# Kernel tuning notes

Hardware: AMD Instinct MI355X
Metric: run time of the kernel (lower is better)

The kernel has to match this reference:

```python
import jax, jax.numpy as jnp
import numpy as np

N = 50000
E = 800000
IN_DIM = 128
HID = 128
HEADS = 8
OUT_DIM = 64
LRELU_SLOPE = 0.2


def setup_inputs() -> dict:
    key = jax.random.key(0)
    ks = jax.random.split(key, 10)
    x = jax.random.normal(ks[0], (N, IN_DIM), dtype=jnp.float32)
    edge_index = jax.random.randint(ks[1], (2, E), 0, N, dtype=jnp.int64)
    c1 = HID // HEADS  # 16
    W1 = jax.random.normal(ks[2], (IN_DIM, HID), dtype=jnp.float32) * (1.0 / np.sqrt(IN_DIM))
    as1 = jax.random.normal(ks[3], (HEADS, c1), dtype=jnp.float32) * 0.1
    ad1 = jax.random.normal(ks[4], (HEADS, c1), dtype=jnp.float32) * 0.1
    b1 = jnp.zeros((HID,), dtype=jnp.float32)
    W2 = jax.random.normal(ks[5], (HID, OUT_DIM), dtype=jnp.float32) * (1.0 / np.sqrt(HID))
    as2 = jax.random.normal(ks[6], (1, OUT_DIM), dtype=jnp.float32) * 0.1
    ad2 = jax.random.normal(ks[7], (1, OUT_DIM), dtype=jnp.float32) * 0.1
    b2 = jnp.zeros((OUT_DIM,), dtype=jnp.float32)
    return {"x": x, "edge_index": edge_index, "W1": W1, "as1": as1, "ad1": ad1,
            "b1": b1, "W2": W2, "as2": as2, "ad2": ad2, "b2": b2}


def gat_conv(x, src, dst, W, a_src, a_dst, b, heads, ch, concat):
    n = x.shape[0]
    h = (x @ W).reshape(n, heads, ch)               # [N,H,C]
    alpha_s = jnp.sum(h * a_src, axis=-1)           # [N,H]
    alpha_d = jnp.sum(h * a_dst, axis=-1)           # [N,H]
    e = jax.nn.leaky_relu(alpha_s[src] + alpha_d[dst], LRELU_SLOPE)  # [E,H]
    m = jax.ops.segment_max(e, dst, num_segments=n)  # per-dst max (self-loops guarantee nonempty)
    e = jnp.exp(e - m[dst])
    denom = jax.ops.segment_sum(e, dst, num_segments=n)
    alpha = e / (denom[dst] + 1e-16)                # [E,H]
    msg = h[src] * alpha[:, :, None]                # [E,H,C]
    out = jax.ops.segment_sum(msg, dst, num_segments=n)  # [N,H,C]
    out = out.reshape(n, heads * ch) if concat else out.mean(axis=1)
    return out + b


def reference(x, edge_index, W1, as1, ad1, b1, W2, as2, ad2, b2):
    n = x.shape[0]
    loops = jnp.arange(n, dtype=edge_index.dtype)
    src = jnp.concatenate([edge_index[0], loops])   # PyG GATConv adds self-loops
    dst = jnp.concatenate([edge_index[1], loops])
    # layer 1: GATBlock (dropout is identity at eval), heads=8, concat, ELU
    h = gat_conv(x, src, dst, W1, as1, ad1, b1, HEADS, HID // HEADS, True)
    h = jax.nn.elu(h)
    # final conv: heads=1, concat=False
    out = gat_conv(h, src, dst, W2, as2, ad2, b2, 1, OUT_DIM, False)
    return jax.nn.log_softmax(out, axis=1)
```

## Files before the change

### kernel.cpp

```cpp
#include <hip/hip_runtime.h>
#include <hip/hip_bf16.h>
#include <math.h>

#define IN_DIM 128
#define HID 128
#define HEADS 8
#define OUT_DIM 64
#define SLOPE 0.2f
#define BSHIFT 7
#define BCAP 4096
#define BCAPSHIFT 12
#define EPT 8

typedef short bf16x8 __attribute__((ext_vector_type(8)));
typedef float f32x4 __attribute__((ext_vector_type(4)));

__device__ __forceinline__ float lrelu(float x) { return fmaxf(x, SLOPE * x); }
__device__ __forceinline__ float bf2f(unsigned u) { return __uint_as_float(u << 16); }
__device__ __forceinline__ unsigned short f2bf(float f) {
    unsigned u = __float_as_uint(f);
    return (unsigned short)((u + 0x7FFF + ((u >> 16) & 1)) >> 16);
}

__global__ __launch_bounds__(256) void setup_kernel(
    const float* __restrict__ W1, const float* __restrict__ W2,
    short* __restrict__ w1t, short* __restrict__ w2t, int* __restrict__ gcursor) {
    int t = threadIdx.x;
    int b = blockIdx.x;
    if (b == 96) {
        for (int i = t; i < 512; i += 256) gcursor[i] = 0;
        return;
    }
    if (b < 64) {
        int id = b * 256 + t;
        int n = id >> 7, k = id & 127;
        w1t[id] = (short)f2bf(W1[k * 128 + n]);
    } else {
        int id = (b - 64) * 256 + t;
        int n = id >> 7, k = id & 127;
        w2t[id] = (short)f2bf(W2[k * 64 + n]);
    }
}

__device__ __forceinline__ void bscatter_body(
    int blk, int* smem, const int* __restrict__ idx,
    int* __restrict__ gcursor, unsigned* __restrict__ bucket_buf,
    int E, int N, int NB) {
    int* hist  = smem;
    int* gbase = smem + 512;
    int* lbase = smem + 1024;
    int* wtot  = smem + 1536;
    int* misc  = smem + 1540;
    unsigned* sent = (unsigned*)(smem + 1552);
    unsigned* spos = (unsigned*)(smem + 3600);
    int t = threadIdx.x;
    for (int i = t; i < 512; i += 256) hist[i] = 0;
    if (t == 0) misc[1] = 0;
    __syncthreads();
    {
        int nz = (idx[2 * t + 1] != 0) + (idx[2 * t + 513] != 0);
        if (nz) atomicAdd(&misc[1], nz);
    }
    __syncthreads();
    int flag = (misc[1] > 16) ? 1 : 0;
    int e0 = blk * (256 * EPT);
    int EN = E + N;
    unsigned ent[EPT];
    int bid[EPT];
    int loc[EPT];
#pragma unroll
    for (int k = 0; k < EPT; k++) {
        int e = e0 + k * 256 + t;
        bid[k] = -1;
        if (e < EN) {
            int src, dst;
            if (e < E) {
                if (flag) { src = idx[e]; dst = idx[E + e]; }
                else      { src = idx[2 * e]; dst = idx[2 * (E + e)]; }
            } else {
                src = dst = e - E;
            }
            int b = dst >> BSHIFT;
            bid[k] = b;
            ent[k] = ((unsigned)(dst & ((1 << BSHIFT) - 1)) << 16) | (unsigned)src;
            loc[k] = atomicAdd(&hist[b], 1);
        }
    }
    __syncthreads();
    int i0 = 2 * t;
    int a = hist[i0], b2 = hist[i0 + 1];
    int ps = a + b2;
    int lane = t & 63, w = t >> 6;
    int incl = ps;
#pragma unroll
    for (int off = 1; off < 64; off <<= 1) {
        int u = __shfl_up(incl, off, 64);
        if (lane >= off) incl += u;
    }
    if (lane == 63) wtot[w] = incl;
    __syncthreads();
    int woff = 0;
    for (int k = 0; k < w; k++) woff += wtot[k];
    int ex0 = woff + incl - ps;
    lbase[i0] = ex0;
    lbase[i0 + 1] = ex0 + a;
    if (t == 255) misc[0] = woff + incl;
    for (int i = t; i < 512; i += 256) {
        int c = hist[i];
        gbase[i] = c ? atomicAdd(&gcursor[i], c) : 0;
    }
    __syncthreads();
#pragma unroll
    for (int k = 0; k < EPT; k++) {
        if (bid[k] >= 0) {
            int p = lbase[bid[k]] + loc[k];
            int pib = gbase[bid[k]] + loc[k];
            sent[p] = ent[k];
            spos[p] = (pib < BCAP) ? (((unsigned)bid[k] << BCAPSHIFT) | (unsigned)pib)
                                   : 0xFFFFFFFFu;
        }
    }
    __syncthreads();
    int tot = misc[0];
    for (int i = t; i < tot; i += 256) {
        unsigned sp = spos[i];
        if (sp != 0xFFFFFFFFu) bucket_buf[sp] = sent[i];
    }
}

__device__ __forceinline__ void gemm1_body(
    int blk, char* smemraw, const float* __restrict__ x, const short* __restrict__ w1t,
    const float* __restrict__ a_s, const float* __restrict__ a_d,
    unsigned short* __restrict__ h1g, float* __restrict__ as_n,
    float* __restrict__ ad_n, int N) {
    short* Wt = (short*)smemraw;
    float* hT = (float*)smemraw;
    int t = threadIdx.x;
    const uint4* src = (const uint4*)w1t;
    for (int id = t; id < 128 * 16; id += 256) {
        int n = id >> 4, kg = id & 15;
        *(uint4*)&Wt[n * 128 + ((kg * 8) ^ ((n & 7) << 3))] = src[id];
    }
    __syncthreads();
    int wv = t >> 6, lane = t & 63;
    int m = lane & 15, q = lane >> 4;
    int row = blk * 64 + wv * 16 + m;
    f32x4 acc[8];
#pragma unroll
    for (int j = 0; j < 8; j++) acc[j] = (f32x4){0.f, 0.f, 0.f, 0.f};
    int msw = (m & 7) << 3;
#pragma unroll
    for (int k0 = 0; k0 < 128; k0 += 32) {
        bf16x8 a = {0, 0, 0, 0, 0, 0, 0, 0};
        if (row < N) {
            const float* xp = &x[(size_t)row * 128 + k0 + q * 8];
            float4 u0 = *(const float4*)xp;
            float4 u1 = *(const float4*)(xp + 4);
            a[0] = (short)f2bf(u0.x); a[1] = (short)f2bf(u0.y);
            a[2] = (short)f2bf(u0.z); a[3] = (short)f2bf(u0.w);
            a[4] = (short)f2bf(u1.x); a[5] = (short)f2bf(u1.y);
            a[6] = (short)f2bf(u1.z); a[7] = (short)f2bf(u1.w);
        }
#pragma unroll
        for (int j = 0; j < 8; j++) {
            bf16x8 b = *(const bf16x8*)&Wt[(j * 16 + m) * 128 + ((k0 + q * 8) ^ msw)];
            acc[j] = __builtin_amdgcn_mfma_f32_16x16x32_bf16(a, b, acc[j], 0, 0, 0);
        }
    }
    __syncthreads();
#pragma unroll
    for (int r = 0; r < 4; r++) {
        int rl = wv * 16 + q * 4 + r;
        int sw = ((rl >> 2) & 1) << 4;
        int rb = rl * 128;
#pragma unroll
        for (int j = 0; j < 8; j++)
            hT[rb + ((j * 16 + m) ^ sw)] = acc[j][r];
    }
    __syncthreads();
    int base = blk * 64;
    for (int id = t; id < 1024; id += 256) {
        int rl = id >> 4, c8 = (id & 15) * 8;
        int rg = base + rl;
        if (rg >= N) continue;
        int sw = ((rl >> 2) & 1) << 4;
        float4 u0 = *(const float4*)&hT[rl * 128 + (c8 ^ sw)];
        float4 u1 = *(const float4*)&hT[rl * 128 + ((c8 + 4) ^ sw)];
        uint4 ow;
        ow.x = (unsigned)f2bf(u0.x) | ((unsigned)f2bf(u0.y) << 16);
        ow.y = (unsigned)f2bf(u0.z) | ((unsigned)f2bf(u0.w) << 16);
        ow.z = (unsigned)f2bf(u1.x) | ((unsigned)f2bf(u1.y) << 16);
        ow.w = (unsigned)f2bf(u1.z) | ((unsigned)f2bf(u1.w) << 16);
        *(uint4*)&h1g[(size_t)rg * 128 + c8] = ow;
    }
    for (int it = t; it < 512; it += 256) {
        int rl = it >> 3, hd = it & 7;
        int rg = base + rl;
        int sw = ((rl >> 2) & 1) << 4;
        const float* ap = a_s + hd * 16;
        const float* dp = a_d + hd * 16;
        float s = 0.f, d = 0.f;
#pragma unroll
        for (int p = 0; p < 4; p++) {
            float4 u = *(const float4*)&hT[rl * 128 + ((hd * 16 + p * 4) ^ sw)];
            s += u.x * ap[p * 4] + u.y * ap[p * 4 + 1] + u.z * ap[p * 4 + 2] + u.w * ap[p * 4 + 3];
            d += u.x * dp[p * 4] + u.y * dp[p * 4 + 1] + u.z * dp[p * 4 + 2] + u.w * dp[p * 4 + 3];
        }
        if (rg < N) {
            as_n[(size_t)base * 8 + it] = s;
            ad_n[(size_t)base * 8 + it] = d;
        }
    }
}

__global__ __launch_bounds__(256) void k1_kernel(
    const int* __restrict__ idx, int* __restrict__ gcursor,
    unsigned* __restrict__ bucket_buf,
    const float* __restrict__ x, const short* __restrict__ w1t,
    const float* __restrict__ a_s, const float* __restrict__ a_d,
    unsigned short* __restrict__ h1g, float* __restrict__ as_n,
    float* __restrict__ ad_n, int E, int N, int NB, int GS) {
    __shared__ long long smem[4096];
    if ((int)blockIdx.x < GS)
        bscatter_body(blockIdx.x, (int*)smem, idx, gcursor, bucket_buf, E, N, NB);
    else
        gemm1_body(blockIdx.x - GS, (char*)smem, x, w1t, a_s, a_d, h1g, as_n, ad_n, N);
}

__device__ __forceinline__ void bsort_body(
    int b, const int* __restrict__ gcursor, const unsigned* __restrict__ bucket_buf,
    int* __restrict__ row_start, int* __restrict__ sorted_src, int N, int NB) {
    __shared__ int cnt[128];
    __shared__ int cur[128];
    __shared__ int red[4];
    __shared__ int s_w0;
    __shared__ int srt[BCAP];
    int t = threadIdx.x;
    if (t < 128) cnt[t] = 0;
    int partial = 0;
    for (int i = t; i < b; i += 256) partial += min(gcursor[i], BCAP);
#pragma unroll
    for (int msk = 32; msk > 0; msk >>= 1) partial += __shfl_xor(partial, msk, 64);
    if ((t & 63) == 0) red[t >> 6] = partial;
    __syncthreads();
    int bbase = red[0] + red[1] + red[2] + red[3];
    int c = min(gcursor[b], BCAP);
    const unsigned* buf = bucket_buf + ((size_t)b << BCAPSHIFT);
    for (int i = t; i < c; i += 256)
        atomicAdd(&cnt[(buf[i] >> 16) & 127], 1);
    __syncthreads();
    int v = (t < 128) ? cnt[t] : 0;
    int lane = t & 63;
    int incl = v;
#pragma unroll
    for (int off = 1; off < 64; off <<= 1) {
        int u = __shfl_up(incl, off, 64);
        if (lane >= off) incl += u;
    }
    if (t == 63) s_w0 = incl;
    __syncthreads();
    if (t < 128) {
        int excl = incl - v + ((t >= 64) ? s_w0 : 0);
        cur[t] = excl;
        int node = (b << BSHIFT) + t;
        if (node <= N) row_start[node] = bbase + excl;
    }
    __syncthreads();
    for (int i = t; i < c; i += 256) {
        unsigned e = buf[i];
        int lp = atomicAdd(&cur[(e >> 16) & 127], 1);
        srt[lp] = (int)(e & 0xFFFFu);
    }
    __syncthreads();
    for (int i = t; i < c; i += 256)
        sorted_src[bbase + i] = srt[i];
}

__global__ __launch_bounds__(256) void k2_kernel(
    const int* __restrict__ gcursor, const unsigned* __restrict__ bucket_buf,
    int* __restrict__ row_start, int* __restrict__ sorted_src,
    int N, int NB, int EN) {
    if (blockIdx.x == 0 && threadIdx.x < 16) sorted_src[EN + threadIdx.x] = 0;
    bsort_body(blockIdx.x, gcursor, bucket_buf, row_start, sorted_src, N, NB);
}

__global__ __launch_bounds__(256) void mid_kernel(
    const int* __restrict__ row_start, const int* __restrict__ sorted_src,
    const float* __restrict__ as_n, const float* __restrict__ ad_n,
    const unsigned short* __restrict__ h1g, const float* __restrict__ b1,
    const short* __restrict__ w2t, const float* __restrict__ a_s2,
    const float* __restrict__ a_d2, unsigned short* __restrict__ h2g,
    float* __restrict__ as2n, float* __restrict__ ad2n, int N) {
    __shared__ short hA[64 * 128];
    __shared__ short Wt[64 * 136];
    int t = threadIdx.x;
    const uint4* srcw = (const uint4*)w2t;
    for (int id = t; id < 64 * 16; id += 256) {
        int n = id >> 4, kg = id & 15;
        *(uint4*)&Wt[n * 136 + kg * 8] = srcw[id];
    }
    int lane = t & 63;
    int g = lane >> 4, j = lane & 15;
    int base = blockIdx.x * 64;
    int grp16 = (t >> 6) * 4 + g;
    int e4 = j >> 2;
    int hh = (j & 3) * 2;
    int hd = j >> 1;
    int hsel = hd & 1;
    int wsrc = hd >> 1;
    for (int ni = 0; ni < 4; ni++) {
        int rowl = ni * 16 + grp16;
        int node = base + rowl;
        float acc[8];
#pragma unroll
        for (int k = 0; k < 8; k++) acc[k] = 0.f;
        float denom = 0.f;
        if (node < N) {
            float2 adp = *(const float2*)&ad_n[(size_t)node * 8 + hh];
            int beg = row_start[node], end = row_start[node + 1];
            for (int i = beg; i < end; i += 4) {
                int se = sorted_src[i + e4];
                float2 asp = *(const float2*)&as_n[(size_t)se * 8 + hh];
                float w0 = __expf(lrelu(asp.x + adp.x));
                float w1 = __expf(lrelu(asp.y + adp.y));
                bool val = (i + e4 < end);
                w0 = val ? w0 : 0.f;
                w1 = val ? w1 : 0.f;
#pragma unroll
                for (int e = 0; e < 4; e++) {
                    int sl = e * 4 + wsrc;
                    int sg = __shfl(se, sl, 16);
                    float wa = __shfl(w0, sl, 16);
                    float wb = __shfl(w1, sl, 16);
                    float wv = hsel ? wb : wa;
                    uint4 hv = *(const uint4*)&h1g[(size_t)sg * 128 + j * 8];
                    acc[0] += wv * bf2f(hv.x & 0xffffu);
                    acc[1] += wv * bf2f(hv.x >> 16);
                    acc[2] += wv * bf2f(hv.y & 0xffffu);
                    acc[3] += wv * bf2f(hv.y >> 16);
                    acc[4] += wv * bf2f(hv.z & 0xffffu);
                    acc[5] += wv * bf2f(hv.z >> 16);
                    acc[6] += wv * bf2f(hv.w & 0xffffu);
                    acc[7] += wv * bf2f(hv.w >> 16);
                    denom += wv;
                }
            }
        }
        float inv = 1.f / (denom + 1e-16f);
        int c0 = j * 8;
        unsigned ow[4];
#pragma unroll
        for (int p = 0; p < 4; p++) {
            float v0 = acc[2 * p] * inv + b1[c0 + 2 * p];
            float v1 = acc[2 * p + 1] * inv + b1[c0 + 2 * p + 1];
            v0 = (v0 > 0.f) ? v0 : (__expf(v0) - 1.f);
            v1 = (v1 > 0.f) ? v1 : (__expf(v1) - 1.f);
            ow[p] = (unsigned)f2bf(v0) | ((unsigned)f2bf(v1) << 16);
        }
        uint4 val = (node < N) ? make_uint4(ow[0], ow[1], ow[2], ow[3])
                               : make_uint4(0, 0, 0, 0);
        *(uint4*)&hA[rowl * 128 + ((j * 8) ^ ((rowl & 7) << 3))] = val;
    }
    __syncthreads();
    int wv = t >> 6;
    int m = lane & 15, q = lane >> 4;
    int rowl = wv * 16 + m;
    int rsw = (rowl & 7) << 3;
    f32x4 acc2[4];
#pragma unroll
    for (int j4 = 0; j4 < 4; j4++) acc2[j4] = (f32x4){0.f, 0.f, 0.f, 0.f};
#pragma unroll
    for (int k0 = 0; k0 < 128; k0 += 32) {
        bf16x8 a = *(const bf16x8*)&hA[rowl * 128 + ((k0 + q * 8) ^ rsw)];
#pragma unroll
        for (int j4 = 0; j4 < 4; j4++) {
            bf16x8 b = *(const bf16x8*)&Wt[(j4 * 16 + m) * 136 + k0 + q * 8];
            acc2[j4] = __builtin_amdgcn_mfma_f32_16x16x32_bf16(a, b, acc2[j4], 0, 0, 0);
        }
    }
    float asl[4], adl[4];
#pragma unroll
    for (int j4 = 0; j4 < 4; j4++) { asl[j4] = a_s2[j4 * 16 + m]; adl[j4] = a_d2[j4 * 16 + m]; }
    int rbase = base + wv * 16 + q * 4;
#pragma unroll
    for (int r = 0; r < 4; r++) {
        int rr = rbase + r;
        float s = 0.f, d = 0.f;
#pragma unroll
        for (int j4 = 0; j4 < 4; j4++) {
            s += acc2[j4][r] * asl[j4];
            d += acc2[j4][r] * adl[j4];
        }
#pragma unroll
        for (int msk = 8; msk > 0; msk >>= 1) {
            s += __shfl_xor(s, msk, 64);
            d += __shfl_xor(d, msk, 64);
        }
        if (rr < N) {
            if (m == 0) { as2n[rr] = s; ad2n[rr] = d; }
#pragma unroll
            for (int j4 = 0; j4 < 4; j4++)
                h2g[(size_t)rr * 64 + j4 * 16 + m] = f2bf(acc2[j4][r]);
        }
    }
}

__global__ __launch_bounds__(256) void agg2_kernel(
    const int* __restrict__ row_start, const int* __restrict__ sorted_src,
    const float* __restrict__ as_n, const float* __restrict__ ad_n,
    const unsigned short* __restrict__ h2g, const float* __restrict__ b2,
    float* __restrict__ out, int N) {
    int lane = threadIdx.x & 63;
    int g = lane >> 4, j = lane & 15;
    int node = blockIdx.x * 16 + (threadIdx.x >> 6) * 4 + g;
    if (node >= N) return;
    int e4 = j >> 2;
    float adv = ad_n[node];
    int beg = row_start[node], end = row_start[node + 1];
    float acc[4];
#pragma unroll
    for (int k = 0; k < 4; k++) acc[k] = 0.f;
    float denom = 0.f;
    for (int i = beg; i < end; i += 4) {
        int se = sorted_src[i + e4];
        float w = __expf(lrelu(as_n[se] + adv));
        w = (i + e4 < end) ? w : 0.f;
#pragma unroll
        for (int e = 0; e < 4; e++) {
            int sg = __shfl(se, e * 4, 16);
            float wvv = __shfl(w, e * 4, 16);
            uint2 hv = *(const uint2*)&h2g[(size_t)sg * 64 + j * 4];
            acc[0] += wvv * bf2f(hv.x & 0xffffu);
            acc[1] += wvv * bf2f(hv.x >> 16);
            acc[2] += wvv * bf2f(hv.y & 0xffffu);
            acc[3] += wvv * bf2f(hv.y >> 16);
            denom += wvv;
        }
    }
    float inv = 1.f / (denom + 1e-16f);
    int c0 = j * 4;
    float v[4];
#pragma unroll
    for (int k = 0; k < 4; k++) v[k] = acc[k] * inv + b2[c0 + k];
    float mx = fmaxf(fmaxf(v[0], v[1]), fmaxf(v[2], v[3]));
#pragma unroll
    for (int msk = 8; msk > 0; msk >>= 1) mx = fmaxf(mx, __shfl_xor(mx, msk, 64));
    float ex = __expf(v[0] - mx) + __expf(v[1] - mx) + __expf(v[2] - mx) + __expf(v[3] - mx);
#pragma unroll
    for (int msk = 8; msk > 0; msk >>= 1) ex += __shfl_xor(ex, msk, 64);
    float lse = mx + __logf(ex);
    *(float4*)&out[(size_t)node * 64 + c0] = make_float4(v[0] - lse, v[1] - lse, v[2] - lse, v[3] - lse);
}

extern "C" void kernel_launch(void* const* d_in, const int* in_sizes, int n_in,
                              void* d_out, int out_size, void* d_ws, size_t ws_size,
                              hipStream_t stream) {
    const float* x   = (const float*)d_in[0];
    const int*   idx = (const int*)d_in[1];
    const float* W1  = (const float*)d_in[2];
    const float* as1 = (const float*)d_in[3];
    const float* ad1 = (const float*)d_in[4];
    const float* b1  = (const float*)d_in[5];
    const float* W2  = (const float*)d_in[6];
    const float* as2 = (const float*)d_in[7];
    const float* ad2 = (const float*)d_in[8];
    const float* b2  = (const float*)d_in[9];
    float* out = (float*)d_out;

    const int N = in_sizes[0] / IN_DIM;
    const int E = in_sizes[1] / 2;
    const int EN = E + N;
    const int NB = (N + (1 << BSHIFT) - 1) >> BSHIFT;
    const int GS = (EN + 256 * EPT - 1) / (256 * EPT);
    const int T1 = (N + 63) / 64;

    unsigned short* h1g   = (unsigned short*)d_ws;
    unsigned short* h1act = h1g + (size_t)N * 128;
    unsigned short* h2g   = h1act + (size_t)N * 128;
    float* as1n = (float*)(h2g + (size_t)N * 64);
    float* ad1n = as1n + (size_t)N * 8;
    float* as2n = ad1n + (size_t)N * 8;
    float* ad2n = as2n + (size_t)N;
    int* row_start  = (int*)(ad2n + (size_t)N);
    int* gcursor    = row_start + N + 1;
    unsigned* bucket_buf = (unsigned*)(gcursor + 512);
    int* sorted_src = (int*)(bucket_buf + ((size_t)NB << BCAPSHIFT));
    short* w1t = (short*)((((uintptr_t)(sorted_src + EN + 16)) + 15) & ~(uintptr_t)15);
    short* w2t = w1t + 128 * 128;
    (void)ws_size; (void)n_in; (void)out_size;

    setup_kernel<<<97, 256, 0, stream>>>(W1, W2, w1t, w2t, gcursor);
    k1_kernel<<<GS + T1, 256, 0, stream>>>(idx, gcursor, bucket_buf,
                                           x, w1t, as1, ad1, h1g, as1n, ad1n, E, N, NB, GS);
    k2_kernel<<<NB, 256, 0, stream>>>(gcursor, bucket_buf, row_start, sorted_src, N, NB, EN);
    mid_kernel<<<T1, 256, 0, stream>>>(row_start, sorted_src, as1n, ad1n, h1g, b1,
                                       w2t, as2, ad2, h2g, as2n, ad2n, N);
    agg2_kernel<<<(N + 15) / 16, 256, 0, stream>>>(row_start, sorted_src, as2n, ad2n, h2g, b2, out, N);
}
```

Measured before the change: 184.5 us.

## Double mid_kernel threads and unroll edge loop by two chunks

```diff
diff --git a/kernel.cpp b/kernel.cpp
--- a/kernel.cpp
+++ b/kernel.cpp
@@ -284,7 +284,7 @@
     bsort_body(blockIdx.x, gcursor, bucket_buf, row_start, sorted_src, N, NB);
 }
 
-__global__ __launch_bounds__(256) void mid_kernel(
+__global__ __launch_bounds__(512) void mid_kernel(
     const int* __restrict__ row_start, const int* __restrict__ sorted_src,
     const float* __restrict__ as_n, const float* __restrict__ ad_n,
     const unsigned short* __restrict__ h1g, const float* __restrict__ b1,
@@ -293,23 +293,25 @@
     float* __restrict__ as2n, float* __restrict__ ad2n, int N) {
     __shared__ short hA[64 * 128];
     __shared__ short Wt[64 * 136];
+    __shared__ float sP[2][64];
+    __shared__ float dP[2][64];
     int t = threadIdx.x;
     const uint4* srcw = (const uint4*)w2t;
-    for (int id = t; id < 64 * 16; id += 256) {
+    for (int id = t; id < 64 * 16; id += 512) {
         int n = id >> 4, kg = id & 15;
         *(uint4*)&Wt[n * 136 + kg * 8] = srcw[id];
     }
     int lane = t & 63;
-    int g = lane >> 4, j = lane & 15;
+    int j = lane & 15;
     int base = blockIdx.x * 64;
-    int grp16 = (t >> 6) * 4 + g;
+    int g32 = (t >> 6) * 4 + (lane >> 4);
     int e4 = j >> 2;
     int hh = (j & 3) * 2;
     int hd = j >> 1;
     int hsel = hd & 1;
     int wsrc = hd >> 1;
-    for (int ni = 0; ni < 4; ni++) {
-        int rowl = ni * 16 + grp16;
+    for (int ni = 0; ni < 2; ni++) {
+        int rowl = ni * 32 + g32;
         int node = base + rowl;
         float acc[8];
 #pragma unroll
@@ -318,20 +320,46 @@
         if (node < N) {
             float2 adp = *(const float2*)&ad_n[(size_t)node * 8 + hh];
             int beg = row_start[node], end = row_start[node + 1];
-            for (int i = beg; i < end; i += 4) {
-                int se = sorted_src[i + e4];
-                float2 asp = *(const float2*)&as_n[(size_t)se * 8 + hh];
-                float w0 = __expf(lrelu(asp.x + adp.x));
-                float w1 = __expf(lrelu(asp.y + adp.y));
-                bool val = (i + e4 < end);
-                w0 = val ? w0 : 0.f;
-                w1 = val ? w1 : 0.f;
+            for (int i = beg; i < end; i += 8) {
+                int i2 = i + 4;
+                int se1 = sorted_src[i + e4];
+                int se2 = (i2 < end) ? sorted_src[i2 + e4] : se1;
+                float2 asp1 = *(const float2*)&as_n[(size_t)se1 * 8 + hh];
+                float2 asp2 = *(const float2*)&as_n[(size_t)se2 * 8 + hh];
+                float w0a = __expf(lrelu(asp1.x + adp.x));
+                float w1a = __expf(lrelu(asp1.y + adp.y));
+                float w0b = __expf(lrelu(asp2.x + adp.x));
+                float w1b = __expf(lrelu(asp2.y + adp.y));
+                bool v1 = (i + e4 < end);
+                bool v2 = (i2 + e4 < end);
+                w0a = v1 ? w0a : 0.f;
+                w1a = v1 ? w1a : 0.f;
+                w0b = v2 ? w0b : 0.f;
+                w1b = v2 ? w1b : 0.f;
 #pragma unroll
                 for (int e = 0; e < 4; e++) {
                     int sl = e * 4 + wsrc;
-                    int sg = __shfl(se, sl, 16);
-                    float wa = __shfl(w0, sl, 16);
-                    float wb = __shfl(w1, sl, 16);
+                    int sg = __shfl(se1, sl, 16);
+                    float wa = __shfl(w0a, sl, 16);
+                    float wb = __shfl(w1a, sl, 16);
+                    float wv = hsel ? wb : wa;
+                    uint4 hv = *(const uint4*)&h1g[(size_t)sg * 128 + j * 8];
+                    acc[0] += wv * bf2f(hv.x & 0xffffu);
+                    acc[1] += wv * bf2f(hv.x >> 16);
+                    acc[2] += wv * bf2f(hv.y & 0xffffu);
+                    acc[3] += wv * bf2f(hv.y >> 16);
+                    acc[4] += wv * bf2f(hv.z & 0xffffu);
+                    acc[5] += wv * bf2f(hv.z >> 16);
+                    acc[6] += wv * bf2f(hv.w & 0xffffu);
+                    acc[7] += wv * bf2f(hv.w >> 16);
+                    denom += wv;
+                }
+#pragma unroll
+                for (int e = 0; e < 4; e++) {
+                    int sl = e * 4 + wsrc;
+                    int sg = __shfl(se2, sl, 16);
+                    float wa = __shfl(w0b, sl, 16);
+                    float wb = __shfl(w1b, sl, 16);
                     float wv = hsel ? wb : wa;
                     uint4 hv = *(const uint4*)&h1g[(size_t)sg * 128 + j * 8];
                     acc[0] += wv * bf2f(hv.x & 0xffffu);
@@ -363,33 +391,40 @@
     }
     __syncthreads();
     int wv = t >> 6;
+    int ch = wv & 1;
+    int rt = wv >> 1;
     int m = lane & 15, q = lane >> 4;
-    int rowl = wv * 16 + m;
+    int rowl = rt * 16 + m;
     int rsw = (rowl & 7) << 3;
-    f32x4 acc2[4];
-#pragma unroll
-    for (int j4 = 0; j4 < 4; j4++) acc2[j4] = (f32x4){0.f, 0.f, 0.f, 0.f};
+    f32x4 acc2[2];
+#pragma unroll
+    for (int jj = 0; jj < 2; jj++) acc2[jj] = (f32x4){0.f, 0.f, 0.f, 0.f};
 #pragma unroll
     for (int k0 = 0; k0 < 128; k0 += 32) {
         bf16x8 a = *(const bf16x8*)&hA[rowl * 128 + ((k0 + q * 8) ^ rsw)];
 #pragma unroll
-        for (int j4 = 0; j4 < 4; j4++) {
+        for (int jj = 0; jj < 2; jj++) {
+            int j4 = ch * 2 + jj;
             bf16x8 b = *(const bf16x8*)&Wt[(j4 * 16 + m) * 136 + k0 + q * 8];
-            acc2[j4] = __builtin_amdgcn_mfma_f32_16x16x32_bf16(a, b, acc2[j4], 0, 0, 0);
-        }
-    }
-    float asl[4], adl[4];
-#pragma unroll
-    for (int j4 = 0; j4 < 4; j4++) { asl[j4] = a_s2[j4 * 16 + m]; adl[j4] = a_d2[j4 * 16 + m]; }
-    int rbase = base + wv * 16 + q * 4;
+            acc2[jj] = __builtin_amdgcn_mfma_f32_16x16x32_bf16(a, b, acc2[jj], 0, 0, 0);
+        }
+    }
+    float asl[2], adl[2];
+#pragma unroll
+    for (int jj = 0; jj < 2; jj++) {
+        asl[jj] = a_s2[(ch * 2 + jj) * 16 + m];
+        adl[jj] = a_d2[(ch * 2 + jj) * 16 + m];
+    }
+    int rb = rt * 16 + q * 4;
 #pragma unroll
     for (int r = 0; r < 4; r++) {
-        int rr = rbase + r;
+        int rl2 = rb + r;
+        int rr = base + rl2;
         float s = 0.f, d = 0.f;
 #pragma unroll
-        for (int j4 = 0; j4 < 4; j4++) {
-            s += acc2[j4][r] * asl[j4];
-            d += acc2[j4][r] * adl[j4];
+        for (int jj = 0; jj < 2; jj++) {
+            s += acc2[jj][r] * asl[jj];
+            d += acc2[jj][r] * adl[jj];
         }
 #pragma unroll
         for (int msk = 8; msk > 0; msk >>= 1) {
@@ -397,10 +432,18 @@
             d += __shfl_xor(d, msk, 64);
         }
         if (rr < N) {
-            if (m == 0) { as2n[rr] = s; ad2n[rr] = d; }
-#pragma unroll
-            for (int j4 = 0; j4 < 4; j4++)
-                h2g[(size_t)rr * 64 + j4 * 16 + m] = f2bf(acc2[j4][r]);
+            if (m == 0) { sP[ch][rl2] = s; dP[ch][rl2] = d; }
+#pragma unroll
+            for (int jj = 0; jj < 2; jj++)
+                h2g[(size_t)rr * 64 + (ch * 2 + jj) * 16 + m] = f2bf(acc2[jj][r]);
+        }
+    }
+    __syncthreads();
+    if (t < 64) {
+        int rr = base + t;
+        if (rr < N) {
+            as2n[rr] = sP[0][t] + sP[1][t];
+            ad2n[rr] = dP[0][t] + dP[1][t];
         }
     }
 }
@@ -493,7 +536,7 @@
     k1_kernel<<<GS + T1, 256, 0, stream>>>(idx, gcursor, bucket_buf,
                                            x, w1t, as1, ad1, h1g, as1n, ad1n, E, N, NB, GS);
     k2_kernel<<<NB, 256, 0, stream>>>(gcursor, bucket_buf, row_start, sorted_src, N, NB, EN);
-    mid_kernel<<<T1, 256, 0, stream>>>(row_start, sorted_src, as1n, ad1n, h1g, b1,
+    mid_kernel<<<T1, 512, 0, stream>>>(row_start, sorted_src, as1n, ad1n, h1g, b1,
                                        w2t, as2, ad2, h2g, as2n, ad2n, N);
     agg2_kernel<<<(N + 15) / 16, 256, 0, stream>>>(row_start, sorted_src, as2n, ad2n, h2g, b2, out, N);
 }
```

Result: no change. 185.7 us (+0.6%).
